# Kernel optimization log

Measured on AMD Instinct MI355X. Metric: run time of the kernel, lower is better.

The kernel has to match this reference:

```python
import jax, jax.numpy as jnp
import numpy as np

HIDDEN = 1024
HEADS = 16
B, L = 2, 2048


def _xavier(key, shape):
    fan_in, fan_out = shape[1], shape[0]
    limit = float(np.sqrt(6.0 / (fan_in + fan_out)))
    return jax.random.uniform(key, shape, jnp.float32, -limit, limit)


def setup_inputs() -> dict:
    key = jax.random.key(0)
    ks = jax.random.split(key, 6)
    return {
        "query": jax.random.normal(ks[0], (B, L, HIDDEN), jnp.float32),
        "bias": jax.random.normal(ks[1], (B, 1, 1, L), jnp.float32),
        "Wq": _xavier(ks[2], (HIDDEN, HIDDEN)), "bq": jnp.zeros((HIDDEN,), jnp.float32),
        "Wk": _xavier(ks[3], (HIDDEN, HIDDEN)), "bk": jnp.zeros((HIDDEN,), jnp.float32),
        "Wv": _xavier(ks[4], (HIDDEN, HIDDEN)), "bv": jnp.zeros((HIDDEN,), jnp.float32),
        "Wo": _xavier(ks[5], (HIDDEN, HIDDEN)), "bo": jnp.zeros((HIDDEN,), jnp.float32),
    }


def _split_heads(x):
    b, l, c = x.shape
    return x.reshape(b, l, HEADS, c // HEADS).transpose(0, 2, 1, 3)  # [B,H,L,d]


def reference(query, bias, Wq, bq, Wk, bk, Wv, bv, Wo, bo):
    d_head = HIDDEN // HEADS
    q = query @ Wq.T + bq
    k = query @ Wk.T + bk
    v = query @ Wv.T + bv
    q = _split_heads(q) * (d_head ** -0.5)  # [B,H,L,d]
    k = _split_heads(k)
    v = _split_heads(v)
    logits = jnp.einsum("bhqd,bhkd->bhqk", q, k) + bias  # [B,H,L,L]
    weights = jax.nn.softmax(logits, axis=-1)
    x = jnp.einsum("bhqk,bhkd->bhqd", weights, v)  # [B,H,L,d]
    x = x.transpose(0, 2, 1, 3).reshape(query.shape[0], query.shape[1], HIDDEN)
    return x @ Wo.T + bo
```

## Files before the change

### kernel.cpp

```cpp
#include <hip/hip_runtime.h>
#include <hip/hip_fp16.h>
#include <stdint.h>

#define HIDDEN 1024
#define HEADS  16
#define DH     64
#define B_     2
#define L_     2048
#define M_TOT  (B_ * L_)
#define ELEMS  (M_TOT * HIDDEN)
#define LOG2E  1.44269504088896340736f

typedef _Float16 f16;
typedef _Float16 f16x4 __attribute__((ext_vector_type(4)));
typedef _Float16 f16x8 __attribute__((ext_vector_type(8)));
typedef float    f32x4 __attribute__((ext_vector_type(4)));
typedef uint32_t u32;
typedef __attribute__((address_space(1))) u32 gu32;
typedef __attribute__((address_space(3))) u32 su32;

#define MFMA16(a, b, c) __builtin_amdgcn_mfma_f32_16x16x16f16(a, b, c, 0, 0, 0)
#define MFMA32(a, b, c) __builtin_amdgcn_mfma_f32_16x16x32_f16(a, b, c, 0, 0, 0)


__global__ __launch_bounds__(256)
void convert_f16(const float* __restrict__ query,
                 const float* __restrict__ Wq, const float* __restrict__ Wk,
                 const float* __restrict__ Wv, const float* __restrict__ Wo,
                 f16* __restrict__ Qh, f16* __restrict__ Wh)
{
    const int NQ4 = ELEMS / 4;
    const int NW4 = (HIDDEN * HIDDEN) / 4;
    const int total = NQ4 + 4 * NW4;
    for (int u = blockIdx.x * 256 + threadIdx.x; u < total; u += gridDim.x * 256) {
        float4 v; f16* dp;
        if (u < NQ4) {
            v = ((const float4*)query)[u];
            dp = Qh + (size_t)u * 4;
        } else {
            const int u2 = u - NQ4;
            const int w = u2 >> 18;
            const int off = u2 & (NW4 - 1);
            const float* W = (w == 0) ? Wq : (w == 1) ? Wk : (w == 2) ? Wv : Wo;
            v = ((const float4*)W)[off];
            dp = Wh + (size_t)u2 * 4;
        }
        f16x4 h = { (f16)v.x, (f16)v.y, (f16)v.z, (f16)v.w };
        *(f16x4*)dp = h;
    }
}

template<int TM, int TN>
__device__ __forceinline__
void gemm_loop(const f16* __restrict__ A, const f16* __restrict__ W,
               int mb, int nb, f32x4 (&acc)[TM / 32][TN / 32])
{
    __shared__ f16 As[2][TM * 32];
    __shared__ f16 Bs[2][TN * 32];

    const int tid  = threadIdx.x;
    const int lane = tid & 63;
    const int wave = tid >> 6;
    const int quad = lane >> 4;
    const int l16  = lane & 15;
    const int wm   = (wave >> 1) * (TM / 2);
    const int wn   = (wave & 1) * (TN / 2);

    constexpr int AISS = TM / 64;
    constexpr int BISS = TN / 64;
    int aoff[AISS], boff[BISS];
#pragma unroll
    for (int q = 0; q < AISS; q++) {
        const int p16 = (wave * AISS + q) * 64 + lane;
        const int r = p16 >> 2;
        const int c8 = (p16 & 3) ^ ((r >> 1) & 3);
        aoff[q] = (mb + r) * HIDDEN + c8 * 8;
    }
#pragma unroll
    for (int q = 0; q < BISS; q++) {
        const int p16 = (wave * BISS + q) * 64 + lane;
        const int r = p16 >> 2;
        const int c8 = (p16 & 3) ^ ((r >> 1) & 3);
        boff[q] = (nb + r) * HIDDEN + c8 * 8;
    }

#pragma unroll
    for (int q = 0; q < AISS; q++)
        __builtin_amdgcn_global_load_lds((gu32*)&A[aoff[q]],
                                         (su32*)&As[0][(wave * AISS + q) * 512], 16, 0, 0);
#pragma unroll
    for (int q = 0; q < BISS; q++)
        __builtin_amdgcn_global_load_lds((gu32*)&W[boff[q]],
                                         (su32*)&Bs[0][(wave * BISS + q) * 512], 16, 0, 0);
    __syncthreads();

    for (int kb = 0; kb < HIDDEN; kb += 32) {
        const int buf = (kb >> 5) & 1;
        const int nkb = (kb + 32 < HIDDEN) ? kb + 32 : 0;

#pragma unroll
        for (int q = 0; q < AISS; q++)
            __builtin_amdgcn_global_load_lds((gu32*)&A[aoff[q] + nkb],
                                             (su32*)&As[buf ^ 1][(wave * AISS + q) * 512], 16, 0, 0);
#pragma unroll
        for (int q = 0; q < BISS; q++)
            __builtin_amdgcn_global_load_lds((gu32*)&W[boff[q] + nkb],
                                             (su32*)&Bs[buf ^ 1][(wave * BISS + q) * 512], 16, 0, 0);

        f16x8 af[TM / 32], bf[TN / 32];
#pragma unroll
        for (int i = 0; i < TM / 32; i++) {
            const int r = wm + i * 16 + l16;
            af[i] = *(const f16x8*)&As[buf][r * 32 + (quad ^ ((r >> 1) & 3)) * 8];
        }
#pragma unroll
        for (int j = 0; j < TN / 32; j++) {
            const int r = wn + j * 16 + l16;
            bf[j] = *(const f16x8*)&Bs[buf][r * 32 + (quad ^ ((r >> 1) & 3)) * 8];
        }
#pragma unroll
        for (int i = 0; i < TM / 32; i++)
#pragma unroll
            for (int j = 0; j < TN / 32; j++)
                acc[i][j] = MFMA32(af[i], bf[j], acc[i][j]);
        __syncthreads();
    }
}

__global__ __launch_bounds__(256)
void proj_qkv(const f16* __restrict__ A, const f16* __restrict__ W,
              const float* __restrict__ bq, const float* __restrict__ bk,
              const float* __restrict__ bv,
              f16* __restrict__ Qo, f16* __restrict__ Ko, f16* __restrict__ Vo)
{
    f32x4 acc[4][4] = {};
    const int mb = blockIdx.x * 128, nb = blockIdx.y * 128;
    gemm_loop<128, 128>(A, W, mb, nb, acc);

    const int lane = threadIdx.x & 63, wave = threadIdx.x >> 6;
    const int quad = lane >> 4, l16 = lane & 15;
    const int wm = (wave >> 1) * 64, wn = (wave & 1) * 64;
    const int nsel = nb >> 10;
    const int nbase = nb & 1023;

    if (nsel < 2) {
        const float* bias = nsel ? bk : bq;
        f16* out = nsel ? Ko : Qo;
        const float scale = nsel ? 1.0f : 0.125f * LOG2E;
#pragma unroll
        for (int i = 0; i < 4; i++)
#pragma unroll
            for (int j = 0; j < 4; j++) {
                const int n1 = nbase + wn + j * 16 + l16;
                const float bn = bias[n1];
                const int h = n1 >> 6, dd = n1 & 63;
#pragma unroll
                for (int r = 0; r < 4; r++) {
                    const int m = mb + wm + i * 16 + quad * 4 + r;
                    const int b = m >> 11, l = m & (L_ - 1);
                    out[(((b * HEADS + h) * L_) + l) * DH + dd] =
                        (f16)((acc[i][j][r] + bn) * scale);
                }
            }
    } else {
#pragma unroll
        for (int i = 0; i < 4; i++)
#pragma unroll
            for (int j = 0; j < 4; j++) {
                const int n1 = nbase + wn + j * 16 + l16;
                const float bn = bv[n1];
                const int h = n1 >> 6, dd = n1 & 63;
                const int m0 = mb + wm + i * 16 + quad * 4;
                const int b = m0 >> 11, l0 = m0 & (L_ - 1);
                f16x4 pk;
#pragma unroll
                for (int r = 0; r < 4; r++) pk[r] = (f16)(acc[i][j][r] + bn);
                *(f16x4*)&Vo[((size_t)(b * HEADS + h) * DH + dd) * L_ + l0] = pk;
            }
    }
}

__global__ __launch_bounds__(256)
void proj_out(const f16* __restrict__ A, const f16* __restrict__ W,
              const float* __restrict__ bo, float* __restrict__ out)
{
    f32x4 acc[4][2] = {};
    const int mb = blockIdx.x * 128, nb = blockIdx.y * 64;
    gemm_loop<128, 64>(A, W, mb, nb, acc);

    const int lane = threadIdx.x & 63, wave = threadIdx.x >> 6;
    const int quad = lane >> 4, l16 = lane & 15;
    const int wm = (wave >> 1) * 64, wn = (wave & 1) * 32;
#pragma unroll
    for (int i = 0; i < 4; i++)
#pragma unroll
        for (int j = 0; j < 2; j++) {
            const int n = nb + wn + j * 16 + l16;
            const float bn = bo[n];
#pragma unroll
            for (int r = 0; r < 4; r++) {
                const int m = mb + wm + i * 16 + quad * 4 + r;
                out[m * HIDDEN + n] = acc[i][j][r] + bn;
            }
        }
}

__global__ __launch_bounds__(256)
void attn(const f16* __restrict__ Q, const f16* __restrict__ K,
          const f16* __restrict__ Vt, const float* __restrict__ bias,
          f16* __restrict__ X)
{
    __shared__ f16 Ks[2][64 * 64];
    __shared__ f16 Vs[2][64 * 64];
    __shared__ float biasl[L_];

    const int tid  = threadIdx.x;
    const int lane = tid & 63;
    const int wave = tid >> 6;
    const int quad = lane >> 4;
    const int l16  = lane & 15;

    const int bh = blockIdx.x >> 4;
    const int b  = bh >> 4, h = bh & 15;
    const int qrow0 = (blockIdx.x & 15) * 128 + wave * 32;

    const f16* Qh  = Q  + (size_t)bh * L_ * DH;
    const f16* Kh  = K  + (size_t)bh * L_ * DH;
    const f16* Vth = Vt + (size_t)bh * DH * L_;

    {
        const float4* bb = (const float4*)(bias + b * L_);
        for (int i = tid; i < L_ / 4; i += 256) {
            const float4 v = bb[i];
            biasl[i * 4 + 0] = v.x * LOG2E;
            biasl[i * 4 + 1] = v.y * LOG2E;
            biasl[i * 4 + 2] = v.z * LOG2E;
            biasl[i * 4 + 3] = v.w * LOG2E;
        }
    }

    int krow[2], kcol[2];
#pragma unroll
    for (int q = 0; q < 2; q++) {
        const int grp = wave * 2 + q;
        const int r = grp * 8 + (lane >> 3);
        const int u = (lane & 7) ^ (r & 7);
        krow[q] = r; kcol[q] = u * 8;
    }

    f16x8 qf[2][2];
#pragma unroll
    for (int qt = 0; qt < 2; qt++)
#pragma unroll
        for (int hh = 0; hh < 2; hh++)
            qf[qt][hh] = *(const f16x8*)&Qh[(qrow0 + qt * 16 + l16) * DH + hh * 32 + quad * 8];

#pragma unroll
    for (int q = 0; q < 2; q++) {
        __builtin_amdgcn_global_load_lds((gu32*)(Kh + (size_t)krow[q] * DH + kcol[q]),
                                         (su32*)&Ks[0][(wave * 2 + q) * 512], 16, 0, 0);
        __builtin_amdgcn_global_load_lds((gu32*)(Vth + (size_t)krow[q] * L_ + kcol[q]),
                                         (su32*)&Vs[0][(wave * 2 + q) * 512], 16, 0, 0);
    }

    f32x4 o[2][4] = {};
    f32x4 osum[2] = {};
    const f16x4 ones = { (f16)1.f, (f16)1.f, (f16)1.f, (f16)1.f };
    __syncthreads();

#pragma unroll 1
    for (int kb = 0; kb < L_; kb += 64) {
        const int buf = (kb >> 6) & 1;
        const int nkb = (kb + 64 < L_) ? kb + 64 : 0;

#pragma unroll
        for (int q = 0; q < 2; q++) {
            __builtin_amdgcn_global_load_lds(
                (gu32*)(Kh + (size_t)(nkb + krow[q]) * DH + kcol[q]),
                (su32*)&Ks[buf ^ 1][(wave * 2 + q) * 512], 16, 0, 0);
            __builtin_amdgcn_global_load_lds(
                (gu32*)(Vth + (size_t)krow[q] * L_ + nkb + kcol[q]),
                (su32*)&Vs[buf ^ 1][(wave * 2 + q) * 512], 16, 0, 0);
        }

#pragma unroll
        for (int c = 0; c < 4; c++) {
            const int krowc = c * 16 + l16;
            const f16x8 ka0 = *(const f16x8*)&Ks[buf][krowc * 64 + (quad ^ (krowc & 7)) * 8];
            const f16x8 ka1 = *(const f16x8*)&Ks[buf][krowc * 64 + ((quad + 4) ^ (krowc & 7)) * 8];
            f16x4 va[4];
#pragma unroll
            for (int t = 0; t < 4; t++) {
                const int vr = t * 16 + l16;
                const int uu = (c * 2 + (quad >> 1)) ^ (vr & 7);
                va[t] = *(const f16x4*)&Vs[buf][vr * 64 + uu * 8 + (quad & 1) * 4];
            }
            const f32x4 blv = *(const f32x4*)&biasl[kb + c * 16 + quad * 4];

#pragma unroll
            for (int qt = 0; qt < 2; qt++) {
                f32x4 z = blv;
                z = MFMA32(ka0, qf[qt][0], z);
                z = MFMA32(ka1, qf[qt][1], z);
                const f16x4 pb = { (f16)__builtin_amdgcn_exp2f(z[0]),
                                   (f16)__builtin_amdgcn_exp2f(z[1]),
                                   (f16)__builtin_amdgcn_exp2f(z[2]),
                                   (f16)__builtin_amdgcn_exp2f(z[3]) };
#pragma unroll
                for (int t = 0; t < 4; t++)
                    o[qt][t] = MFMA16(va[t], pb, o[qt][t]);
                osum[qt] = MFMA16(ones, pb, osum[qt]);
            }
        }
        __syncthreads();
    }

#pragma unroll
    for (int qt = 0; qt < 2; qt++) {
        const float inv = 1.0f / osum[qt][0];
        const size_t qrow = (size_t)b * L_ + qrow0 + qt * 16 + l16;
#pragma unroll
        for (int t = 0; t < 4; t++) {
            f16x4 pk;
#pragma unroll
            for (int r = 0; r < 4; r++) pk[r] = (f16)(o[qt][t][r] * inv);
            *(f16x4*)&X[qrow * HIDDEN + h * DH + t * 16 + quad * 4] = pk;
        }
    }
}

extern "C" void kernel_launch(void* const* d_in, const int* in_sizes, int n_in,
                              void* d_out, int out_size, void* d_ws, size_t ws_size,
                              hipStream_t stream)
{
    const float* query = (const float*)d_in[0];
    const float* bias  = (const float*)d_in[1];
    const float* Wq = (const float*)d_in[2]; const float* bq = (const float*)d_in[3];
    const float* Wk = (const float*)d_in[4]; const float* bk = (const float*)d_in[5];
    const float* Wv = (const float*)d_in[6]; const float* bv = (const float*)d_in[7];
    const float* Wo = (const float*)d_in[8]; const float* bo = (const float*)d_in[9];
    float* out = (float*)d_out;

    f16* Wh = (f16*)d_ws;
    f16* Qh = Wh + 4096 * 1024;
    f16* Kf = Qh + ELEMS;
    f16* Vf = Kf + ELEMS;
    f16* Qf = Vf + ELEMS;
    f16* Xf = Qh;

    convert_f16<<<2048, 256, 0, stream>>>(query, Wq, Wk, Wv, Wo, Qh, Wh);
    proj_qkv<<<dim3(32, 24), 256, 0, stream>>>(Qh, Wh, bq, bk, bv, Qf, Kf, Vf);
    attn<<<512, 256, 0, stream>>>(Qf, Kf, Vf, bias, Xf);
    proj_out<<<dim3(32, 16), 256, 0, stream>>>(Xf, Wh + 3072 * 1024, bo, out);
}
```

Baseline: 207.1 us.

## Halve query rows per attention block and read bias directly from global

Each attention block now covers 64 query rows (16 per wave) instead of 128, doubling the grid to 1024 blocks so more blocks run per CU at once. The shared-memory bias staging is removed; bias is read from global memory each iteration and scaled by log2(e) inline. Each block now streams its own full K/V for 64 rather than 128 queries, so total K/V traffic doubles. Each loaded K/V tile also feeds fewer MFMAs, and the repeated global bias loads add latency inside the inner loop.

```diff
diff --git a/kernel.cpp b/kernel.cpp
--- a/kernel.cpp
+++ b/kernel.cpp
@@ -212,7 +212,6 @@
 {
     __shared__ f16 Ks[2][64 * 64];
     __shared__ f16 Vs[2][64 * 64];
-    __shared__ float biasl[L_];
 
     const int tid  = threadIdx.x;
     const int lane = tid & 63;
@@ -220,24 +219,14 @@
     const int quad = lane >> 4;
     const int l16  = lane & 15;
 
-    const int bh = blockIdx.x >> 4;
+    const int bh = blockIdx.x >> 5;
     const int b  = bh >> 4, h = bh & 15;
-    const int qrow0 = (blockIdx.x & 15) * 128 + wave * 32;
+    const int qrow0 = (blockIdx.x & 31) * 64 + wave * 16;
 
     const f16* Qh  = Q  + (size_t)bh * L_ * DH;
     const f16* Kh  = K  + (size_t)bh * L_ * DH;
     const f16* Vth = Vt + (size_t)bh * DH * L_;
-
-    {
-        const float4* bb = (const float4*)(bias + b * L_);
-        for (int i = tid; i < L_ / 4; i += 256) {
-            const float4 v = bb[i];
-            biasl[i * 4 + 0] = v.x * LOG2E;
-            biasl[i * 4 + 1] = v.y * LOG2E;
-            biasl[i * 4 + 2] = v.z * LOG2E;
-            biasl[i * 4 + 3] = v.w * LOG2E;
-        }
-    }
+    const float* biasb = bias + b * L_;
 
     int krow[2], kcol[2];
 #pragma unroll
@@ -248,12 +237,8 @@
         krow[q] = r; kcol[q] = u * 8;
     }
 
-    f16x8 qf[2][2];
-#pragma unroll
-    for (int qt = 0; qt < 2; qt++)
-#pragma unroll
-        for (int hh = 0; hh < 2; hh++)
-            qf[qt][hh] = *(const f16x8*)&Qh[(qrow0 + qt * 16 + l16) * DH + hh * 32 + quad * 8];
+    f16x8 qf0 = *(const f16x8*)&Qh[(qrow0 + l16) * DH + quad * 8];
+    f16x8 qf1 = *(const f16x8*)&Qh[(qrow0 + l16) * DH + 32 + quad * 8];
 
 #pragma unroll
     for (int q = 0; q < 2; q++) {
@@ -263,8 +248,8 @@
                                          (su32*)&Vs[0][(wave * 2 + q) * 512], 16, 0, 0);
     }
 
-    f32x4 o[2][4] = {};
-    f32x4 osum[2] = {};
+    f32x4 o[4] = {};
+    f32x4 osum = {};
     const f16x4 ones = { (f16)1.f, (f16)1.f, (f16)1.f, (f16)1.f };
     __syncthreads();
 
@@ -295,37 +280,32 @@
                 const int uu = (c * 2 + (quad >> 1)) ^ (vr & 7);
                 va[t] = *(const f16x4*)&Vs[buf][vr * 64 + uu * 8 + (quad & 1) * 4];
             }
-            const f32x4 blv = *(const f32x4*)&biasl[kb + c * 16 + quad * 4];
-
-#pragma unroll
-            for (int qt = 0; qt < 2; qt++) {
-                f32x4 z = blv;
-                z = MFMA32(ka0, qf[qt][0], z);
-                z = MFMA32(ka1, qf[qt][1], z);
-                const f16x4 pb = { (f16)__builtin_amdgcn_exp2f(z[0]),
-                                   (f16)__builtin_amdgcn_exp2f(z[1]),
-                                   (f16)__builtin_amdgcn_exp2f(z[2]),
-                                   (f16)__builtin_amdgcn_exp2f(z[3]) };
-#pragma unroll
-                for (int t = 0; t < 4; t++)
-                    o[qt][t] = MFMA16(va[t], pb, o[qt][t]);
-                osum[qt] = MFMA16(ones, pb, osum[qt]);
-            }
+            const f32x4 blv = *(const f32x4*)&biasb[kb + c * 16 + quad * 4];
+
+            f32x4 z = { blv[0] * LOG2E, blv[1] * LOG2E,
+                        blv[2] * LOG2E, blv[3] * LOG2E };
+            z = MFMA32(ka0, qf0, z);
+            z = MFMA32(ka1, qf1, z);
+            const f16x4 pb = { (f16)__builtin_amdgcn_exp2f(z[0]),
+                               (f16)__builtin_amdgcn_exp2f(z[1]),
+                               (f16)__builtin_amdgcn_exp2f(z[2]),
+                               (f16)__builtin_amdgcn_exp2f(z[3]) };
+#pragma unroll
+            for (int t = 0; t < 4; t++)
+                o[t] = MFMA16(va[t], pb, o[t]);
+            osum = MFMA16(ones, pb, osum);
         }
         __syncthreads();
     }
 
-#pragma unroll
-    for (int qt = 0; qt < 2; qt++) {
-        const float inv = 1.0f / osum[qt][0];
-        const size_t qrow = (size_t)b * L_ + qrow0 + qt * 16 + l16;
-#pragma unroll
-        for (int t = 0; t < 4; t++) {
-            f16x4 pk;
-#pragma unroll
-            for (int r = 0; r < 4; r++) pk[r] = (f16)(o[qt][t][r] * inv);
-            *(f16x4*)&X[qrow * HIDDEN + h * DH + t * 16 + quad * 4] = pk;
-        }
+    const float inv = 1.0f / osum[0];
+    const size_t qrow = (size_t)b * L_ + qrow0 + l16;
+#pragma unroll
+    for (int t = 0; t < 4; t++) {
+        f16x4 pk;
+#pragma unroll
+        for (int r = 0; r < 4; r++) pk[r] = (f16)(o[t][r] * inv);
+        *(f16x4*)&X[qrow * HIDDEN + h * DH + t * 16 + quad * 4] = pk;
     }
 }
 
@@ -350,6 +330,6 @@
 
     convert_f16<<<2048, 256, 0, stream>>>(query, Wq, Wk, Wv, Wo, Qh, Wh);
     proj_qkv<<<dim3(32, 24), 256, 0, stream>>>(Qh, Wh, bq, bk, bv, Qf, Kf, Vf);
-    attn<<<512, 256, 0, stream>>>(Qf, Kf, Vf, bias, Xf);
+    attn<<<1024, 256, 0, stream>>>(Qf, Kf, Vf, bias, Xf);
     proj_out<<<dim3(32, 16), 256, 0, stream>>>(Xf, Wh + 3072 * 1024, bo, out);
 }
```

After: 219.6 us. +6.0%, slower.
